# Kernel optimization log

Hardware: AMD Instinct MI355X
Metric: run time of the kernel (lower is better)

## Reference

```python
import jax, jax.numpy as jnp
import numpy as np
import math

B, N, D, H, F = 2, 2048, 512, 8, 2048
DH = D // H
LN_EPS = 1e-5
PHASE_ALPHA = 0.1


def _layernorm(x, g, b):
    mu = jnp.mean(x, axis=-1, keepdims=True)
    var = jnp.mean(jnp.square(x - mu), axis=-1, keepdims=True)
    return (x - mu) * jax.lax.rsqrt(var + LN_EPS) * g + b


def setup_inputs() -> dict:
    key = jax.random.key(0)
    ks = jax.random.split(key, 16)
    s = 0.02
    return {
        "h": jax.random.normal(ks[0], (B, N, D), dtype=jnp.float32),
        "phases": jax.random.normal(ks[1], (B, N, H), dtype=jnp.float32),
        "mask": jnp.zeros((B, N), dtype=bool),
        "Wq": jax.random.normal(ks[2], (D, D), dtype=jnp.float32) * s,
        "Wk": jax.random.normal(ks[3], (D, D), dtype=jnp.float32) * s,
        "Wp": jax.random.normal(ks[4], (D, H), dtype=jnp.float32) * s,
        "bp": jnp.zeros((H,), dtype=jnp.float32),
        "Wv": jax.random.normal(ks[5], (D, D), dtype=jnp.float32) * s,
        "Wo": jax.random.normal(ks[6], (D, D), dtype=jnp.float32) * s,
        "W1": jax.random.normal(ks[7], (D, F), dtype=jnp.float32) * s,
        "b1": jnp.zeros((F,), dtype=jnp.float32),
        "W2": jax.random.normal(ks[8], (F, D), dtype=jnp.float32) * s,
        "b2": jnp.zeros((D,), dtype=jnp.float32),
        "g1": jnp.ones((D,), dtype=jnp.float32),
        "be1": jnp.zeros((D,), dtype=jnp.float32),
        "g2": jnp.ones((D,), dtype=jnp.float32),
        "be2": jnp.zeros((D,), dtype=jnp.float32),
        "Wph": jax.random.normal(ks[9], (D, H), dtype=jnp.float32) * s,
        "bph": jnp.zeros((H,), dtype=jnp.float32),
    }


def reference(h, phases, mask, Wq, Wk, Wp, bp, Wv, Wo, W1, b1, W2, b2, g1, be1, g2, be2, Wph, bph):
    # --- HarmonicEdgeLayer ---
    Q = (h @ Wq).reshape(B, N, H, DH)  # (B,N,H,dh)
    K = (h @ Wk).reshape(B, N, H, DH)
    scores = jnp.einsum("bnhd,bmhd->bhnm", Q, K) / math.sqrt(DH)  # (B,H,N,N)
    ph = h @ Wp + bp                       # (B,N,H)
    phi = jnp.transpose(ph, (0, 2, 1))     # (B,H,N)
    harmonic = jnp.cos(phi[:, :, :, None] - phi[:, :, None, :])  # (B,H,N,N)
    scores = scores * (1.0 + harmonic) * 0.5
    scores = jnp.where(mask[:, None, None, :], -jnp.inf, scores)
    edge_weights = jax.nn.softmax(scores, axis=-1)  # (B,H,N,N)

    # --- HarmonicNodeUpdate ---
    V = (h @ Wv).reshape(B, N, H, DH)
    messages = jnp.einsum("bhnm,bmhd->bnhd", edge_weights, V).reshape(B, N, D)
    messages = messages @ Wo
    h1 = _layernorm(h + messages, g1, be1)
    ffn = jax.nn.gelu(h1 @ W1 + b1, approximate=False) @ W2 + b2
    h2 = _layernorm(h1 + ffn, g2, be2)

    # --- PhaseUpdate ---
    phases_new = phases + PHASE_ALPHA * jnp.tanh(h2 @ Wph + bph) * math.pi

    # convergence metric
    delta = jnp.mean(jnp.linalg.norm(h2 - h, axis=-1))
    return h2, phases_new, delta
```

## Files before the change

### kernel.cpp

```cpp
#include <hip/hip_runtime.h>
#include <math.h>

#define BB 2
#define NN 2048
#define DD 512
#define HH 8
#define DHH 64
#define FF 2048
#define MROWS (BB*NN)
#define LN_EPS 1e-5f
#define PHASE_ALPHA 0.1f
#define PI_F 3.14159265358979323846f
#define SCALE 0.125f

typedef __attribute__((ext_vector_type(8))) short  bf16x8;
typedef __attribute__((ext_vector_type(4))) float  f32x4;
typedef __attribute__((ext_vector_type(4))) unsigned short us4;

__device__ __forceinline__ unsigned short f2bf(float x) {
    unsigned int u = __float_as_uint(x);
    u += 0x7fffu + ((u >> 16) & 1u);
    return (unsigned short)(u >> 16);
}

__global__ __launch_bounds__(256) void convert_bf16_kernel(
    const float* __restrict__ X, unsigned short* __restrict__ Y, int n8)
{
    int i = blockIdx.x*256 + threadIdx.x;
    if (i >= n8) return;
    const float4 a = *(const float4*)&X[i*8];
    const float4 b = *(const float4*)&X[i*8 + 4];
    uint4 o;
    o.x = (unsigned)f2bf(a.x) | ((unsigned)f2bf(a.y) << 16);
    o.y = (unsigned)f2bf(a.z) | ((unsigned)f2bf(a.w) << 16);
    o.z = (unsigned)f2bf(b.x) | ((unsigned)f2bf(b.y) << 16);
    o.w = (unsigned)f2bf(b.z) | ((unsigned)f2bf(b.w) << 16);
    *(uint4*)&Y[i*8] = o;
}

__global__ __launch_bounds__(256) void wtrans_kernel(
    const float* __restrict__ W, unsigned short* __restrict__ WT, int K, int N)
{
    __shared__ unsigned short T[32][33];
    const int k0 = blockIdx.y*32, n0 = blockIdx.x*32;
    const int r = threadIdx.x >> 3, cc = (threadIdx.x & 7)*4;
    float4 v = *(const float4*)&W[(size_t)(k0 + r)*N + n0 + cc];
    T[cc+0][r] = f2bf(v.x); T[cc+1][r] = f2bf(v.y);
    T[cc+2][r] = f2bf(v.z); T[cc+3][r] = f2bf(v.w);
    __syncthreads();
    us4 o; o.x = T[r][cc]; o.y = T[r][cc+1]; o.z = T[r][cc+2]; o.w = T[r][cc+3];
    *(us4*)&WT[(size_t)(n0 + r)*K + k0 + cc] = o;
}

__global__ __launch_bounds__(256) void vtrans_kernel(
    const unsigned short* __restrict__ Vb, unsigned short* __restrict__ VT)
{
    __shared__ unsigned short T[32][33];
    const int b = blockIdx.z;
    const int n0 = blockIdx.x*32, c0 = blockIdx.y*32;
    const int r = threadIdx.x >> 3, cc = (threadIdx.x & 7)*4;
    us4 v = *(const us4*)&Vb[((size_t)b*NN + n0 + r)*DD + c0 + cc];
    T[cc+0][r] = v.x; T[cc+1][r] = v.y; T[cc+2][r] = v.z; T[cc+3][r] = v.w;
    __syncthreads();
    const int cg = c0 + r;
    const int hh = cg >> 6, dh = cg & 63;
    us4 o; o.x = T[r][cc]; o.y = T[r][cc+1]; o.z = T[r][cc+2]; o.w = T[r][cc+3];
    *(us4*)&VT[(((size_t)b*HH + hh)*DHH + dh)*NN + n0 + cc] = o;
}

template<int OUTBF16, int BIAS, int ACT>
__global__ __launch_bounds__(256, 2) void mfma_gemm(
    const unsigned short* __restrict__ A, const unsigned short* __restrict__ BT,
    const float* __restrict__ bias, void* __restrict__ Cout,
    int M, int Nc, int K)
{
    __shared__ unsigned short As[128][72];
    __shared__ unsigned short Bs[128][72];

    const int tid = threadIdx.x;
    const int w = tid >> 6, lane = tid & 63;
    const int c = lane & 15, g = lane >> 4;
    const int wr = w >> 1, wc = w & 1;
    const int bm = blockIdx.y*128, bn = blockIdx.x*128;
    const int lrow = tid >> 3, lkc = (tid & 7)*8;

    const int NT = K / 64;
    f32x4 zero = {0.f, 0.f, 0.f, 0.f};
    f32x4 acc[4][4];
    #pragma unroll
    for (int i = 0; i < 4; ++i)
        #pragma unroll
        for (int j = 0; j < 4; ++j) acc[i][j] = zero;

    uint4 pa[4], pb[4];
    #pragma unroll
    for (int p = 0; p < 4; ++p) {
        pa[p] = *(const uint4*)&A [(size_t)(bm + lrow + p*32)*K + lkc];
        pb[p] = *(const uint4*)&BT[(size_t)(bn + lrow + p*32)*K + lkc];
    }

    for (int kt = 0; kt < NT; ++kt) {
        __syncthreads();
        #pragma unroll
        for (int p = 0; p < 4; ++p) {
            *(uint4*)&As[lrow + p*32][lkc] = pa[p];
            *(uint4*)&Bs[lrow + p*32][lkc] = pb[p];
        }
        __syncthreads();
        if (kt + 1 < NT) {
            #pragma unroll
            for (int p = 0; p < 4; ++p) {
                pa[p] = *(const uint4*)&A [(size_t)(bm + lrow + p*32)*K + (kt+1)*64 + lkc];
                pb[p] = *(const uint4*)&BT[(size_t)(bn + lrow + p*32)*K + (kt+1)*64 + lkc];
            }
        }
        #pragma unroll
        for (int ks = 0; ks < 2; ++ks) {
            bf16x8 af[4], bf[4];
            #pragma unroll
            for (int mf = 0; mf < 4; ++mf)
                af[mf] = *(const bf16x8*)&As[wr*64 + mf*16 + c][ks*32 + g*8];
            #pragma unroll
            for (int nf = 0; nf < 4; ++nf)
                bf[nf] = *(const bf16x8*)&Bs[wc*64 + nf*16 + c][ks*32 + g*8];
            #pragma unroll
            for (int mf = 0; mf < 4; ++mf)
                #pragma unroll
                for (int nf = 0; nf < 4; ++nf)
                    acc[mf][nf] = __builtin_amdgcn_mfma_f32_16x16x32_bf16(
                        af[mf], bf[nf], acc[mf][nf], 0, 0, 0);
        }
    }

    #pragma unroll
    for (int mf = 0; mf < 4; ++mf)
        #pragma unroll
        for (int nf = 0; nf < 4; ++nf) {
            const int col = bn + wc*64 + nf*16 + c;
            const float bv = BIAS ? bias[col] : 0.f;
            #pragma unroll
            for (int r = 0; r < 4; ++r) {
                const int row = bm + wr*64 + mf*16 + g*4 + r;
                float x = acc[mf][nf][r] + bv;
                if (ACT == 1) x = 0.5f * x * (1.f + erff(x * 0.70710678118654752f));
                if (OUTBF16) ((unsigned short*)Cout)[(size_t)row*Nc + col] = f2bf(x);
                else         ((float*)Cout)[(size_t)row*Nc + col] = x;
            }
        }
}

__global__ __launch_bounds__(256) void phase_proj_kernel(
    const float* __restrict__ X, const float* __restrict__ Wp,
    const float* __restrict__ bp, float* __restrict__ cosPt, float* __restrict__ sinPt)
{
    __shared__ float Wl[DD*HH];
    for (int i = threadIdx.x; i < DD*HH; i += 256) Wl[i] = Wp[i];
    __syncthreads();
    int row = blockIdx.x*32 + (threadIdx.x >> 3);
    int hh  = threadIdx.x & 7;
    const float* xr = X + (size_t)row * DD;
    float acc = bp[hh];
    for (int k = 0; k < DD; k += 4) {
        float4 xv = *(const float4*)&xr[k];
        acc += xv.x*Wl[(k  )*HH+hh] + xv.y*Wl[(k+1)*HH+hh]
             + xv.z*Wl[(k+2)*HH+hh] + xv.w*Wl[(k+3)*HH+hh];
    }
    const int b = row >> 11, n = row & (NN-1);
    cosPt[((size_t)b*HH + hh)*NN + n] = cosf(acc);
    sinPt[((size_t)b*HH + hh)*NN + n] = sinf(acc);
}

__global__ __launch_bounds__(256) void phase_update_kernel(
    const float* __restrict__ H2, const float* __restrict__ Wph,
    const float* __restrict__ bph, const float* __restrict__ phases,
    float* __restrict__ phases_out)
{
    __shared__ float Wl[DD*HH];
    for (int i = threadIdx.x; i < DD*HH; i += 256) Wl[i] = Wph[i];
    __syncthreads();
    int row = blockIdx.x*32 + (threadIdx.x >> 3);
    int hh  = threadIdx.x & 7;
    const float* xr = H2 + (size_t)row * DD;
    float acc = bph[hh];
    for (int k = 0; k < DD; k += 4) {
        float4 xv = *(const float4*)&xr[k];
        acc += xv.x*Wl[(k  )*HH+hh] + xv.y*Wl[(k+1)*HH+hh]
             + xv.z*Wl[(k+2)*HH+hh] + xv.w*Wl[(k+3)*HH+hh];
    }
    phases_out[row*HH + hh] = phases[row*HH + hh] + PHASE_ALPHA * tanhf(acc) * PI_F;
}

__global__ __launch_bounds__(256, 2) void attn_kernel(
    const unsigned short* __restrict__ Qb, const unsigned short* __restrict__ Kb,
    const unsigned short* __restrict__ VT,
    const float* __restrict__ cosPt, const float* __restrict__ sinPt,
    const unsigned char* __restrict__ mask, unsigned short* __restrict__ msgb)
{
    __shared__ float Os[64][68];
    __shared__ float MwS[4][64], LwS[4][64];
    __shared__ unsigned short Pl[4][64][40];

    const int tid = threadIdx.x;
    const int w = tid >> 6, lane = tid & 63;
    const int c = lane & 15, g = lane >> 4;
    const int qBase = blockIdx.x * 64;
    const int hh = blockIdx.y, b = blockIdx.z;
    const size_t rowOff = (size_t)b * NN;
    const int bh = b*HH + hh;
    const size_t cosBase = (size_t)bh * NN;

    for (int i = tid; i < 64*68; i += 256) ((float*)Os)[i] = 0.f;

    bf16x8 qf[4][2];
    #pragma unroll
    for (int nf = 0; nf < 4; ++nf)
        #pragma unroll
        for (int ks = 0; ks < 2; ++ks)
            qf[nf][ks] = *(const bf16x8*)&Qb[(rowOff + qBase + nf*16 + c)*DD
                                             + hh*DHH + ks*32 + g*8];
    float cq[4], sq[4];
    #pragma unroll
    for (int nf = 0; nf < 4; ++nf) {
        cq[nf] = cosPt[cosBase + qBase + nf*16 + c];
        sq[nf] = sinPt[cosBase + qBase + nf*16 + c];
    }

    f32x4 zero = {0.f, 0.f, 0.f, 0.f};
    f32x4 acc[4][4];
    #pragma unroll
    for (int i = 0; i < 4; ++i)
        #pragma unroll
        for (int j = 0; j < 4; ++j) acc[i][j] = zero;
    float mst[4], lst[4];
    #pragma unroll
    for (int i = 0; i < 4; ++i) { mst[i] = -INFINITY; lst[i] = 0.f; }

    __syncthreads();

    for (int s = w; s < NN/32; s += 4) {
        const int kb0 = s * 32;
        f32x4 st[2][4];
        #pragma unroll
        for (int mf = 0; mf < 2; ++mf) {
            bf16x8 kf0 = *(const bf16x8*)&Kb[(rowOff + kb0 + mf*16 + c)*DD + hh*DHH + g*8];
            bf16x8 kf1 = *(const bf16x8*)&Kb[(rowOff + kb0 + mf*16 + c)*DD + hh*DHH + 32 + g*8];
            #pragma unroll
            for (int nf = 0; nf < 4; ++nf) {
                st[mf][nf] = __builtin_amdgcn_mfma_f32_16x16x32_bf16(kf0, qf[nf][0], zero, 0, 0, 0);
                st[mf][nf] = __builtin_amdgcn_mfma_f32_16x16x32_bf16(kf1, qf[nf][1], st[mf][nf], 0, 0, 0);
            }
        }
        #pragma unroll
        for (int mf = 0; mf < 2; ++mf) {
            const int keyb = kb0 + mf*16 + g*4;
            const f32x4 ck = *(const f32x4*)&cosPt[cosBase + keyb];
            const f32x4 sk = *(const f32x4*)&sinPt[cosBase + keyb];
            const unsigned int mk = *(const unsigned int*)&mask[rowOff + keyb];
            #pragma unroll
            for (int nf = 0; nf < 4; ++nf)
                #pragma unroll
                for (int r = 0; r < 4; ++r) {
                    float wgt = 0.5f + 0.5f*(cq[nf]*ck[r] + sq[nf]*sk[r]);
                    float v = st[mf][nf][r] * SCALE * wgt;
                    st[mf][nf][r] = ((mk >> (8*r)) & 0xff) ? -INFINITY : v;
                }
        }
        #pragma unroll
        for (int nf = 0; nf < 4; ++nf) {
            float tmax = -INFINITY;
            #pragma unroll
            for (int mf = 0; mf < 2; ++mf)
                #pragma unroll
                for (int r = 0; r < 4; ++r) tmax = fmaxf(tmax, st[mf][nf][r]);
            tmax = fmaxf(tmax, __shfl_xor(tmax, 16));
            tmax = fmaxf(tmax, __shfl_xor(tmax, 32));
            const float mnew = fmaxf(mst[nf], tmax);
            const float corr = (mst[nf] == -INFINITY) ? 0.f : __expf(mst[nf] - mnew);
            float psum = 0.f;
            unsigned short* prow = &Pl[w][nf*16 + c][0];
            #pragma unroll
            for (int mf = 0; mf < 2; ++mf) {
                float p0 = __expf(st[mf][nf][0] - mnew);
                float p1 = __expf(st[mf][nf][1] - mnew);
                float p2 = __expf(st[mf][nf][2] - mnew);
                float p3 = __expf(st[mf][nf][3] - mnew);
                psum += (p0 + p1) + (p2 + p3);
                *(unsigned int*)&prow[mf*16 + g*4    ] = (unsigned)f2bf(p0) | ((unsigned)f2bf(p1) << 16);
                *(unsigned int*)&prow[mf*16 + g*4 + 2] = (unsigned)f2bf(p2) | ((unsigned)f2bf(p3) << 16);
            }
            psum += __shfl_xor(psum, 16);
            psum += __shfl_xor(psum, 32);
            lst[nf] = lst[nf]*corr + psum;
            mst[nf] = mnew;
            #pragma unroll
            for (int mo = 0; mo < 4; ++mo)
                #pragma unroll
                for (int r = 0; r < 4; ++r) acc[mo][nf][r] *= corr;
        }
        bf16x8 vf[4], pf[4];
        #pragma unroll
        for (int mo = 0; mo < 4; ++mo)
            vf[mo] = *(const bf16x8*)&VT[((size_t)bh*DHH + mo*16 + c)*NN + kb0 + g*8];
        #pragma unroll
        for (int nf = 0; nf < 4; ++nf)
            pf[nf] = *(const bf16x8*)&Pl[w][nf*16 + c][g*8];
        #pragma unroll
        for (int mo = 0; mo < 4; ++mo)
            #pragma unroll
            for (int nf = 0; nf < 4; ++nf)
                acc[mo][nf] = __builtin_amdgcn_mfma_f32_16x16x32_bf16(
                    vf[mo], pf[nf], acc[mo][nf], 0, 0, 0);
    }

    if (lane < 16) {
        #pragma unroll
        for (int nf = 0; nf < 4; ++nf) {
            MwS[w][nf*16 + lane] = mst[nf];
            LwS[w][nf*16 + lane] = lst[nf];
        }
    }
    __syncthreads();
    float fac[4];
    #pragma unroll
    for (int nf = 0; nf < 4; ++nf) {
        const int q = nf*16 + c;
        float M = fmaxf(fmaxf(MwS[0][q], MwS[1][q]), fmaxf(MwS[2][q], MwS[3][q]));
        float L = LwS[0][q]*__expf(MwS[0][q]-M) + LwS[1][q]*__expf(MwS[1][q]-M)
                + LwS[2][q]*__expf(MwS[2][q]-M) + LwS[3][q]*__expf(MwS[3][q]-M);
        fac[nf] = __expf(mst[nf] - M) / L;
    }
    #pragma unroll
    for (int mo = 0; mo < 4; ++mo)
        #pragma unroll
        for (int nf = 0; nf < 4; ++nf)
            #pragma unroll
            for (int r = 0; r < 4; ++r)
                atomicAdd(&Os[mo*16 + g*4 + r][nf*16 + c], acc[mo][nf][r] * fac[nf]);
    __syncthreads();

    const int q = tid >> 2, dh0 = (tid & 3) * 16;
    unsigned int ov[8];
    #pragma unroll
    for (int i = 0; i < 8; ++i)
        ov[i] = (unsigned)f2bf(Os[dh0 + 2*i][q]) | ((unsigned)f2bf(Os[dh0 + 2*i + 1][q]) << 16);
    unsigned short* op = &msgb[(rowOff + qBase + q)*DD + hh*DHH + dh0];
    *(uint4*)&op[0] = *(uint4*)&ov[0];
    *(uint4*)&op[8] = *(uint4*)&ov[4];
}

template<int WITH_DELTA, int WBF16>
__global__ __launch_bounds__(256) void ln_kernel(
    const float* __restrict__ x, const float* __restrict__ y,
    const float* __restrict__ g, const float* __restrict__ bvec,
    float* __restrict__ out, unsigned short* __restrict__ outb,
    const float* __restrict__ href, float* __restrict__ deltaAcc)
{
    const int row = blockIdx.x;
    const int tid = threadIdx.x;
    const size_t base = (size_t)row * DD + tid*2;
    float2 xv = *(const float2*)(x + base);
    float2 yv = *(const float2*)(y + base);
    float v0 = xv.x + yv.x;
    float v1 = xv.y + yv.y;
    float s  = v0 + v1;
    float sq = v0*v0 + v1*v1;
    #pragma unroll
    for (int m = 1; m < 64; m <<= 1) {
        s  += __shfl_xor(s,  m, 64);
        sq += __shfl_xor(sq, m, 64);
    }
    __shared__ float redS[4], redQ[4];
    int wv = tid >> 6;
    if ((tid & 63) == 0) { redS[wv] = s; redQ[wv] = sq; }
    __syncthreads();
    s  = redS[0] + redS[1] + redS[2] + redS[3];
    sq = redQ[0] + redQ[1] + redQ[2] + redQ[3];
    float mu  = s * (1.f/DD);
    float var = sq * (1.f/DD) - mu*mu;
    float inv = rsqrtf(var + LN_EPS);
    float o0 = (v0 - mu)*inv*g[tid*2  ] + bvec[tid*2  ];
    float o1 = (v1 - mu)*inv*g[tid*2+1] + bvec[tid*2+1];
    float2 ov; ov.x = o0; ov.y = o1;
    *(float2*)(out + base) = ov;
    if (WBF16)
        ((unsigned int*)outb)[(size_t)row*(DD/2) + tid] =
            (unsigned)f2bf(o0) | ((unsigned)f2bf(o1) << 16);

    if (WITH_DELTA) {
        float d0 = o0 - href[base], d1 = o1 - href[base + 1];
        float ds = d0*d0 + d1*d1;
        #pragma unroll
        for (int m = 1; m < 64; m <<= 1) ds += __shfl_xor(ds, m, 64);
        __shared__ float redD[4];
        if ((tid & 63) == 0) redD[wv] = ds;
        __syncthreads();
        if (tid == 0) {
            float t = redD[0] + redD[1] + redD[2] + redD[3];
            atomicAdd(deltaAcc, sqrtf(t));
        }
    }
}

__global__ void delta_finalize(const float* __restrict__ acc, float* __restrict__ out)
{
    out[0] = acc[0] * (1.f / (float)MROWS);
}

extern "C" void kernel_launch(void* const* d_in, const int* in_sizes, int n_in,
                              void* d_out, int out_size, void* d_ws, size_t ws_size,
                              hipStream_t stream)
{
    (void)in_sizes; (void)n_in; (void)out_size; (void)ws_size;
    const float* h      = (const float*)d_in[0];
    const float* phases = (const float*)d_in[1];
    const unsigned char* mask = (const unsigned char*)d_in[2];
    const float* Wq  = (const float*)d_in[3];
    const float* Wk  = (const float*)d_in[4];
    const float* Wp  = (const float*)d_in[5];
    const float* bp  = (const float*)d_in[6];
    const float* Wv  = (const float*)d_in[7];
    const float* Wo  = (const float*)d_in[8];
    const float* W1  = (const float*)d_in[9];
    const float* b1  = (const float*)d_in[10];
    const float* W2  = (const float*)d_in[11];
    const float* b2  = (const float*)d_in[12];
    const float* g1  = (const float*)d_in[13];
    const float* be1 = (const float*)d_in[14];
    const float* g2  = (const float*)d_in[15];
    const float* be2 = (const float*)d_in[16];
    const float* Wph = (const float*)d_in[17];
    const float* bph = (const float*)d_in[18];

    char* ws = (char*)d_ws;
    const size_t MB = 1024*1024;
    unsigned short* hb   = (unsigned short*)(ws);
    unsigned short* WqT  = (unsigned short*)(ws + 4*MB);
    unsigned short* WkT  = (unsigned short*)(ws + 4*MB + 512*1024);
    unsigned short* WvT  = (unsigned short*)(ws + 5*MB);
    unsigned short* WoT  = (unsigned short*)(ws + 5*MB + 512*1024);
    unsigned short* W1T  = (unsigned short*)(ws + 6*MB);
    unsigned short* W2T  = (unsigned short*)(ws + 8*MB);
    unsigned short* Qb   = (unsigned short*)(ws + 10*MB);
    unsigned short* Kb   = (unsigned short*)(ws + 14*MB);
    unsigned short* Vb   = (unsigned short*)(ws + 18*MB);
    unsigned short* VT   = (unsigned short*)(ws + 22*MB);
    unsigned short* T1b  = Qb;
    unsigned short* msgb = (unsigned short*)(ws + 26*MB);
    float* mo    = (float*)(ws + 30*MB);
    float* ffn   = mo;
    float* h1    = (float*)(ws + 38*MB);
    unsigned short* h1b = (unsigned short*)(ws + 46*MB);
    float* cosPt = (float*)(ws + 50*MB);
    float* sinPt = (float*)(ws + 50*MB + 64*1024);
    float* dAcc  = (float*)(ws + 50*MB + 128*1024);

    float* out_h2    = (float*)d_out;
    float* out_ph    = out_h2 + (size_t)MROWS*DD;
    float* out_delta = out_ph + MROWS*HH;

    hipMemsetAsync(dAcc, 0, sizeof(float), stream);

    dim3 blk(256);
    convert_bf16_kernel<<<dim3(MROWS*DD/8/256), blk, 0, stream>>>(h, hb, MROWS*DD/8);
    wtrans_kernel<<<dim3(DD/32, DD/32), blk, 0, stream>>>(Wq, WqT, DD, DD);
    wtrans_kernel<<<dim3(DD/32, DD/32), blk, 0, stream>>>(Wk, WkT, DD, DD);
    wtrans_kernel<<<dim3(DD/32, DD/32), blk, 0, stream>>>(Wv, WvT, DD, DD);
    wtrans_kernel<<<dim3(DD/32, DD/32), blk, 0, stream>>>(Wo, WoT, DD, DD);
    wtrans_kernel<<<dim3(FF/32, DD/32), blk, 0, stream>>>(W1, W1T, DD, FF);
    wtrans_kernel<<<dim3(DD/32, FF/32), blk, 0, stream>>>(W2, W2T, FF, DD);
    phase_proj_kernel<<<dim3(MROWS/32), blk, 0, stream>>>(h, Wp, bp, cosPt, sinPt);
    mfma_gemm<1,0,0><<<dim3(DD/128, MROWS/128), blk, 0, stream>>>(hb, WqT, nullptr, Qb, MROWS, DD, DD);
    mfma_gemm<1,0,0><<<dim3(DD/128, MROWS/128), blk, 0, stream>>>(hb, WkT, nullptr, Kb, MROWS, DD, DD);
    mfma_gemm<1,0,0><<<dim3(DD/128, MROWS/128), blk, 0, stream>>>(hb, WvT, nullptr, Vb, MROWS, DD, DD);
    vtrans_kernel<<<dim3(NN/32, DD/32, BB), blk, 0, stream>>>(Vb, VT);
    attn_kernel<<<dim3(NN/64, HH, BB), blk, 0, stream>>>(Qb, Kb, VT, cosPt, sinPt, mask, msgb);
    mfma_gemm<0,0,0><<<dim3(DD/128, MROWS/128), blk, 0, stream>>>(msgb, WoT, nullptr, mo, MROWS, DD, DD);
    ln_kernel<0,1><<<dim3(MROWS), blk, 0, stream>>>(h, mo, g1, be1, h1, h1b, nullptr, nullptr);
    mfma_gemm<1,1,1><<<dim3(FF/128, MROWS/128), blk, 0, stream>>>(h1b, W1T, b1, T1b, MROWS, FF, DD);
    mfma_gemm<0,1,0><<<dim3(DD/128, MROWS/128), blk, 0, stream>>>(T1b, W2T, b2, ffn, MROWS, DD, FF);
    ln_kernel<1,0><<<dim3(MROWS), blk, 0, stream>>>(h1, ffn, g2, be2, out_h2, nullptr, h, dAcc);
    phase_update_kernel<<<dim3(MROWS/32), blk, 0, stream>>>(out_h2, Wph, bph, phases, out_ph);
    delta_finalize<<<dim3(1), dim3(1), 0, stream>>>(dAcc, out_delta);
}
```

Baseline: 614.4 us.

## Fuse QKV projections into one GEMM and retile with split-K for W2

The three Q/K/V projections become a single GEMM against the contiguous transposed weights, writing an interleaved [M,3D] buffer that the attention and V-transpose kernels now index with a 3D leading dimension. The GEMM template gains configurable BM/BN tiles and a split-K mode with atomic float accumulation. It is used with smaller 64x64 tiles for the narrow Wo GEMM and with 2-way split-K for the K=2048 W2 GEMM, whose b2 bias moves into the following layernorm. The aim is fewer launches, more blocks to fill the CUs on the narrow GEMMs, and shared loads of h. In exchange it adds a memset plus atomic traffic, and the floating-point summation order is no longer deterministic.

```diff
diff --git a/kernel.cpp b/kernel.cpp
--- a/kernel.cpp
+++ b/kernel.cpp
@@ -12,6 +12,7 @@
 #define PHASE_ALPHA 0.1f
 #define PI_F 3.14159265358979323846f
 #define SCALE 0.125f
+#define QLD (3*DD)
 
 typedef __attribute__((ext_vector_type(8))) short  bf16x8;
 typedef __attribute__((ext_vector_type(4))) float  f32x4;
@@ -53,13 +54,13 @@
 }
 
 __global__ __launch_bounds__(256) void vtrans_kernel(
-    const unsigned short* __restrict__ Vb, unsigned short* __restrict__ VT)
+    const unsigned short* __restrict__ qkv, unsigned short* __restrict__ VT)
 {
     __shared__ unsigned short T[32][33];
     const int b = blockIdx.z;
     const int n0 = blockIdx.x*32, c0 = blockIdx.y*32;
     const int r = threadIdx.x >> 3, cc = (threadIdx.x & 7)*4;
-    us4 v = *(const us4*)&Vb[((size_t)b*NN + n0 + r)*DD + c0 + cc];
+    us4 v = *(const us4*)&qkv[((size_t)b*NN + n0 + r)*QLD + 2*DD + c0 + cc];
     T[cc+0][r] = v.x; T[cc+1][r] = v.y; T[cc+2][r] = v.z; T[cc+3][r] = v.w;
     __syncthreads();
     const int cg = c0 + r;
@@ -68,83 +69,93 @@
     *(us4*)&VT[(((size_t)b*HH + hh)*DHH + dh)*NN + n0 + cc] = o;
 }
 
-template<int OUTBF16, int BIAS, int ACT>
+template<int BM, int BN, int SPLITK, int OUTBF16, int BIAS, int ACT, int ATOMIC>
 __global__ __launch_bounds__(256, 2) void mfma_gemm(
     const unsigned short* __restrict__ A, const unsigned short* __restrict__ BT,
     const float* __restrict__ bias, void* __restrict__ Cout,
     int M, int Nc, int K)
 {
-    __shared__ unsigned short As[128][72];
-    __shared__ unsigned short Bs[128][72];
+    constexpr int FM = BM/32, FN = BN/32;
+    constexpr int ROWS = BM + BN;
+    constexpr int NLOAD = ROWS*8/256;
+    __shared__ unsigned short Ss[ROWS][72];
 
     const int tid = threadIdx.x;
     const int w = tid >> 6, lane = tid & 63;
     const int c = lane & 15, g = lane >> 4;
     const int wr = w >> 1, wc = w & 1;
-    const int bm = blockIdx.y*128, bn = blockIdx.x*128;
-    const int lrow = tid >> 3, lkc = (tid & 7)*8;
-
-    const int NT = K / 64;
+    const int bm = blockIdx.y*BM, bn = blockIdx.x*BN;
+    const int k0 = (SPLITK > 1) ? blockIdx.z * (K / SPLITK) : 0;
+    const int NT = (K / SPLITK) / 64;
+
     f32x4 zero = {0.f, 0.f, 0.f, 0.f};
-    f32x4 acc[4][4];
-    #pragma unroll
-    for (int i = 0; i < 4; ++i)
-        #pragma unroll
-        for (int j = 0; j < 4; ++j) acc[i][j] = zero;
-
-    uint4 pa[4], pb[4];
-    #pragma unroll
-    for (int p = 0; p < 4; ++p) {
-        pa[p] = *(const uint4*)&A [(size_t)(bm + lrow + p*32)*K + lkc];
-        pb[p] = *(const uint4*)&BT[(size_t)(bn + lrow + p*32)*K + lkc];
+    f32x4 acc[FM][FN];
+    #pragma unroll
+    for (int i = 0; i < FM; ++i)
+        #pragma unroll
+        for (int j = 0; j < FN; ++j) acc[i][j] = zero;
+
+    uint4 pf[NLOAD];
+    #pragma unroll
+    for (int l = 0; l < NLOAD; ++l) {
+        const int i = tid + l*256;
+        const int r = i >> 3, kc = (i & 7)*8;
+        const unsigned short* src = (r < BM) ? &A [(size_t)(bm + r)*K + k0 + kc]
+                                             : &BT[(size_t)(bn + r - BM)*K + k0 + kc];
+        pf[l] = *(const uint4*)src;
     }
 
     for (int kt = 0; kt < NT; ++kt) {
         __syncthreads();
         #pragma unroll
-        for (int p = 0; p < 4; ++p) {
-            *(uint4*)&As[lrow + p*32][lkc] = pa[p];
-            *(uint4*)&Bs[lrow + p*32][lkc] = pb[p];
+        for (int l = 0; l < NLOAD; ++l) {
+            const int i = tid + l*256;
+            *(uint4*)&Ss[i >> 3][(i & 7)*8] = pf[l];
         }
         __syncthreads();
         if (kt + 1 < NT) {
             #pragma unroll
-            for (int p = 0; p < 4; ++p) {
-                pa[p] = *(const uint4*)&A [(size_t)(bm + lrow + p*32)*K + (kt+1)*64 + lkc];
-                pb[p] = *(const uint4*)&BT[(size_t)(bn + lrow + p*32)*K + (kt+1)*64 + lkc];
+            for (int l = 0; l < NLOAD; ++l) {
+                const int i = tid + l*256;
+                const int r = i >> 3, kc = (i & 7)*8;
+                const unsigned short* src = (r < BM)
+                    ? &A [(size_t)(bm + r)*K + k0 + (kt+1)*64 + kc]
+                    : &BT[(size_t)(bn + r - BM)*K + k0 + (kt+1)*64 + kc];
+                pf[l] = *(const uint4*)src;
             }
         }
         #pragma unroll
         for (int ks = 0; ks < 2; ++ks) {
-            bf16x8 af[4], bf[4];
-            #pragma unroll
-            for (int mf = 0; mf < 4; ++mf)
-                af[mf] = *(const bf16x8*)&As[wr*64 + mf*16 + c][ks*32 + g*8];
-            #pragma unroll
-            for (int nf = 0; nf < 4; ++nf)
-                bf[nf] = *(const bf16x8*)&Bs[wc*64 + nf*16 + c][ks*32 + g*8];
-            #pragma unroll
-            for (int mf = 0; mf < 4; ++mf)
+            bf16x8 af[FM], bfr[FN];
+            #pragma unroll
+            for (int mf = 0; mf < FM; ++mf)
+                af[mf] = *(const bf16x8*)&Ss[wr*(BM/2) + mf*16 + c][ks*32 + g*8];
+            #pragma unroll
+            for (int nf = 0; nf < FN; ++nf)
+                bfr[nf] = *(const bf16x8*)&Ss[BM + wc*(BN/2) + nf*16 + c][ks*32 + g*8];
+            #pragma unroll
+            for (int mf = 0; mf < FM; ++mf)
                 #pragma unroll
-                for (int nf = 0; nf < 4; ++nf)
+                for (int nf = 0; nf < FN; ++nf)
                     acc[mf][nf] = __builtin_amdgcn_mfma_f32_16x16x32_bf16(
-                        af[mf], bf[nf], acc[mf][nf], 0, 0, 0);
-        }
-    }
-
-    #pragma unroll
-    for (int mf = 0; mf < 4; ++mf)
-        #pragma unroll
-        for (int nf = 0; nf < 4; ++nf) {
-            const int col = bn + wc*64 + nf*16 + c;
+                        af[mf], bfr[nf], acc[mf][nf], 0, 0, 0);
+        }
+    }
+
+    #pragma unroll
+    for (int mf = 0; mf < FM; ++mf)
+        #pragma unroll
+        for (int nf = 0; nf < FN; ++nf) {
+            const int col = bn + wc*(BN/2) + nf*16 + c;
             const float bv = BIAS ? bias[col] : 0.f;
             #pragma unroll
             for (int r = 0; r < 4; ++r) {
-                const int row = bm + wr*64 + mf*16 + g*4 + r;
+                const int row = bm + wr*(BM/2) + mf*16 + g*4 + r;
                 float x = acc[mf][nf][r] + bv;
                 if (ACT == 1) x = 0.5f * x * (1.f + erff(x * 0.70710678118654752f));
-                if (OUTBF16) ((unsigned short*)Cout)[(size_t)row*Nc + col] = f2bf(x);
-                else         ((float*)Cout)[(size_t)row*Nc + col] = x;
+                if (ATOMIC)       atomicAdd(&((float*)Cout)[(size_t)row*Nc + col], x);
+                else if (OUTBF16) ((unsigned short*)Cout)[(size_t)row*Nc + col] = f2bf(x);
+                else              ((float*)Cout)[(size_t)row*Nc + col] = x;
             }
         }
 }
@@ -191,8 +202,7 @@
 }
 
 __global__ __launch_bounds__(256, 2) void attn_kernel(
-    const unsigned short* __restrict__ Qb, const unsigned short* __restrict__ Kb,
-    const unsigned short* __restrict__ VT,
+    const unsigned short* __restrict__ qkv, const unsigned short* __restrict__ VT,
     const float* __restrict__ cosPt, const float* __restrict__ sinPt,
     const unsigned char* __restrict__ mask, unsigned short* __restrict__ msgb)
 {
@@ -216,8 +226,8 @@
     for (int nf = 0; nf < 4; ++nf)
         #pragma unroll
         for (int ks = 0; ks < 2; ++ks)
-            qf[nf][ks] = *(const bf16x8*)&Qb[(rowOff + qBase + nf*16 + c)*DD
-                                             + hh*DHH + ks*32 + g*8];
+            qf[nf][ks] = *(const bf16x8*)&qkv[(rowOff + qBase + nf*16 + c)*QLD
+                                              + hh*DHH + ks*32 + g*8];
     float cq[4], sq[4];
     #pragma unroll
     for (int nf = 0; nf < 4; ++nf) {
@@ -242,8 +252,8 @@
         f32x4 st[2][4];
         #pragma unroll
         for (int mf = 0; mf < 2; ++mf) {
-            bf16x8 kf0 = *(const bf16x8*)&Kb[(rowOff + kb0 + mf*16 + c)*DD + hh*DHH + g*8];
-            bf16x8 kf1 = *(const bf16x8*)&Kb[(rowOff + kb0 + mf*16 + c)*DD + hh*DHH + 32 + g*8];
+            bf16x8 kf0 = *(const bf16x8*)&qkv[(rowOff + kb0 + mf*16 + c)*QLD + DD + hh*DHH + g*8];
+            bf16x8 kf1 = *(const bf16x8*)&qkv[(rowOff + kb0 + mf*16 + c)*QLD + DD + hh*DHH + 32 + g*8];
             #pragma unroll
             for (int nf = 0; nf < 4; ++nf) {
                 st[mf][nf] = __builtin_amdgcn_mfma_f32_16x16x32_bf16(kf0, qf[nf][0], zero, 0, 0, 0);
@@ -297,19 +307,19 @@
                 #pragma unroll
                 for (int r = 0; r < 4; ++r) acc[mo][nf][r] *= corr;
         }
-        bf16x8 vf[4], pf[4];
+        bf16x8 vf[4], pfr[4];
         #pragma unroll
         for (int mo = 0; mo < 4; ++mo)
             vf[mo] = *(const bf16x8*)&VT[((size_t)bh*DHH + mo*16 + c)*NN + kb0 + g*8];
         #pragma unroll
         for (int nf = 0; nf < 4; ++nf)
-            pf[nf] = *(const bf16x8*)&Pl[w][nf*16 + c][g*8];
+            pfr[nf] = *(const bf16x8*)&Pl[w][nf*16 + c][g*8];
         #pragma unroll
         for (int mo = 0; mo < 4; ++mo)
             #pragma unroll
             for (int nf = 0; nf < 4; ++nf)
                 acc[mo][nf] = __builtin_amdgcn_mfma_f32_16x16x32_bf16(
-                    vf[mo], pf[nf], acc[mo][nf], 0, 0, 0);
+                    vf[mo], pfr[nf], acc[mo][nf], 0, 0, 0);
     }
 
     if (lane < 16) {
@@ -348,10 +358,11 @@
     *(uint4*)&op[8] = *(uint4*)&ov[4];
 }
 
-template<int WITH_DELTA, int WBF16>
+template<int WITH_DELTA, int WBF16, int YBIAS>
 __global__ __launch_bounds__(256) void ln_kernel(
     const float* __restrict__ x, const float* __restrict__ y,
     const float* __restrict__ g, const float* __restrict__ bvec,
+    const float* __restrict__ ybias,
     float* __restrict__ out, unsigned short* __restrict__ outb,
     const float* __restrict__ href, float* __restrict__ deltaAcc)
 {
@@ -362,6 +373,7 @@
     float2 yv = *(const float2*)(y + base);
     float v0 = xv.x + yv.x;
     float v1 = xv.y + yv.y;
+    if (YBIAS) { v0 += ybias[tid*2]; v1 += ybias[tid*2+1]; }
     float s  = v0 + v1;
     float sq = v0*v0 + v1*v1;
     #pragma unroll
@@ -440,11 +452,9 @@
     unsigned short* WoT  = (unsigned short*)(ws + 5*MB + 512*1024);
     unsigned short* W1T  = (unsigned short*)(ws + 6*MB);
     unsigned short* W2T  = (unsigned short*)(ws + 8*MB);
-    unsigned short* Qb   = (unsigned short*)(ws + 10*MB);
-    unsigned short* Kb   = (unsigned short*)(ws + 14*MB);
-    unsigned short* Vb   = (unsigned short*)(ws + 18*MB);
+    unsigned short* qkvb = (unsigned short*)(ws + 10*MB);
     unsigned short* VT   = (unsigned short*)(ws + 22*MB);
-    unsigned short* T1b  = Qb;
+    unsigned short* T1b  = qkvb;
     unsigned short* msgb = (unsigned short*)(ws + 26*MB);
     float* mo    = (float*)(ws + 30*MB);
     float* ffn   = mo;
@@ -469,16 +479,19 @@
     wtrans_kernel<<<dim3(FF/32, DD/32), blk, 0, stream>>>(W1, W1T, DD, FF);
     wtrans_kernel<<<dim3(DD/32, FF/32), blk, 0, stream>>>(W2, W2T, FF, DD);
     phase_proj_kernel<<<dim3(MROWS/32), blk, 0, stream>>>(h, Wp, bp, cosPt, sinPt);
-    mfma_gemm<1,0,0><<<dim3(DD/128, MROWS/128), blk, 0, stream>>>(hb, WqT, nullptr, Qb, MROWS, DD, DD);
-    mfma_gemm<1,0,0><<<dim3(DD/128, MROWS/128), blk, 0, stream>>>(hb, WkT, nullptr, Kb, MROWS, DD, DD);
-    mfma_gemm<1,0,0><<<dim3(DD/128, MROWS/128), blk, 0, stream>>>(hb, WvT, nullptr, Vb, MROWS, DD, DD);
-    vtrans_kernel<<<dim3(NN/32, DD/32, BB), blk, 0, stream>>>(Vb, VT);
-    attn_kernel<<<dim3(NN/64, HH, BB), blk, 0, stream>>>(Qb, Kb, VT, cosPt, sinPt, mask, msgb);
-    mfma_gemm<0,0,0><<<dim3(DD/128, MROWS/128), blk, 0, stream>>>(msgb, WoT, nullptr, mo, MROWS, DD, DD);
-    ln_kernel<0,1><<<dim3(MROWS), blk, 0, stream>>>(h, mo, g1, be1, h1, h1b, nullptr, nullptr);
-    mfma_gemm<1,1,1><<<dim3(FF/128, MROWS/128), blk, 0, stream>>>(h1b, W1T, b1, T1b, MROWS, FF, DD);
-    mfma_gemm<0,1,0><<<dim3(DD/128, MROWS/128), blk, 0, stream>>>(T1b, W2T, b2, ffn, MROWS, DD, FF);
-    ln_kernel<1,0><<<dim3(MROWS), blk, 0, stream>>>(h1, ffn, g2, be2, out_h2, nullptr, h, dAcc);
+    mfma_gemm<64,128,1,1,0,0,0><<<dim3((3*DD)/128, MROWS/64), blk, 0, stream>>>(
+        hb, WqT, nullptr, qkvb, MROWS, 3*DD, DD);
+    vtrans_kernel<<<dim3(NN/32, DD/32, BB), blk, 0, stream>>>(qkvb, VT);
+    attn_kernel<<<dim3(NN/64, HH, BB), blk, 0, stream>>>(qkvb, VT, cosPt, sinPt, mask, msgb);
+    mfma_gemm<64,64,1,0,0,0,0><<<dim3(DD/64, MROWS/64), blk, 0, stream>>>(
+        msgb, WoT, nullptr, mo, MROWS, DD, DD);
+    ln_kernel<0,1,0><<<dim3(MROWS), blk, 0, stream>>>(h, mo, g1, be1, nullptr, h1, h1b, nullptr, nullptr);
+    mfma_gemm<128,128,1,1,1,1,0><<<dim3(FF/128, MROWS/128), blk, 0, stream>>>(
+        h1b, W1T, b1, T1b, MROWS, FF, DD);
+    hipMemsetAsync(ffn, 0, (size_t)MROWS*DD*sizeof(float), stream);
+    mfma_gemm<64,64,2,0,0,0,1><<<dim3(DD/64, MROWS/64, 2), blk, 0, stream>>>(
+        T1b, W2T, nullptr, ffn, MROWS, DD, FF);
+    ln_kernel<1,0,1><<<dim3(MROWS), blk, 0, stream>>>(h1, ffn, g2, be2, b2, out_h2, nullptr, h, dAcc);
     phase_update_kernel<<<dim3(MROWS/32), blk, 0, stream>>>(out_h2, Wph, bph, phases, out_ph);
     delta_finalize<<<dim3(1), dim3(1), 0, stream>>>(dAcc, out_delta);
 }
```

Result: faster. 511.5 us (-16.8%).
